# Kernel optimization log

Hardware: AMD Instinct MI355X
Metric: run time of the kernel (lower is better)

Reference implementation:

```python
import jax, jax.numpy as jnp
import numpy as np

B, N, C, H = 4, 1024, 512, 8
HD = C // H
SCALE = HD ** -0.5
LN_EPS = 1e-5


def setup_inputs() -> dict:
    key = jax.random.key(0)
    ks = jax.random.split(key, 4)
    return {
        "x": jax.random.normal(ks[0], (B, N, C), dtype=jnp.float32),
        "Wqkv": jax.random.normal(ks[1], (C, 3 * C), dtype=jnp.float32) * (C ** -0.5),
        "bqkv": jnp.zeros((3 * C,), dtype=jnp.float32),
        "order_weights": jnp.ones((3,), dtype=jnp.float32),
        "Wproj": jax.random.normal(ks[2], (C, C), dtype=jnp.float32) * (C ** -0.5),
        "bproj": jnp.zeros((C,), dtype=jnp.float32),
        "gamma": jnp.ones((C,), dtype=jnp.float32),
        "beta": jnp.zeros((C,), dtype=jnp.float32),
    }


def reference(x, Wqkv, bqkv, order_weights, Wproj, bproj, gamma, beta):
    b, n, c = x.shape
    qkv = (x @ Wqkv + bqkv).reshape(b, n, 3, H, HD)
    qkv = jnp.transpose(qkv, (2, 0, 3, 1, 4))  # [3, B, H, N, HD]
    q, k, v = qkv[0], qkv[1], qkv[2]

    base = jnp.einsum('bhnd,bhmd->bhnm', q, k) * SCALE  # [B, H, N, N]

    ow = jax.nn.softmax(order_weights)
    # torch loop: term_0 = base, term_i = base**(i+1)
    attn = ow[0] * base
    cur = base
    for i in range(1, order_weights.shape[0]):
        cur = cur * base
        attn = attn + ow[i] * cur

    attn_final = jax.nn.softmax(attn, axis=-1)

    out = jnp.einsum('bhnm,bhmd->bhnd', attn_final, v)
    out = jnp.transpose(out, (0, 2, 1, 3)).reshape(b, n, c)
    out = out @ Wproj + bproj

    y = x + out
    mu = jnp.mean(y, axis=-1, keepdims=True)
    var = jnp.var(y, axis=-1, keepdims=True)
    y = (y - mu) / jnp.sqrt(var + LN_EPS) * gamma + beta
    return y, attn_final
```

## Files before the change

kernel.cpp:

```cpp
#include <hip/hip_runtime.h>
#include <math.h>

#define B_ 4
#define N_ 1024
#define C_ 512
#define H_ 8
#define HD_ 64
#define SCALE_ 0.125f
#define LN_EPS_ 1e-5f

typedef _Float16 f16x8 __attribute__((ext_vector_type(8)));
typedef float f32x4 __attribute__((ext_vector_type(4)));

__device__ __forceinline__ void cvt_split(const float4& A, const float4& Bv,
                                          f16x8& hi, f16x8& lo) {
    float v[8] = {A.x, A.y, A.z, A.w, Bv.x, Bv.y, Bv.z, Bv.w};
#pragma unroll
    for (int i = 0; i < 8; ++i) {
        _Float16 h = (_Float16)v[i];
        hi[i] = h;
        lo[i] = (_Float16)(v[i] - (float)h);
    }
}

__global__ __launch_bounds__(256) void qkv_gemm(const float* __restrict__ x,
                                                const float* __restrict__ Wqkv,
                                                const float* __restrict__ bqkv,
                                                float* __restrict__ qkv) {
    const int K = C_;
    const int NN = 3 * C_;
    __shared__ float As[64][17];
    __shared__ float Bs[16][64];

    const int tid = threadIdx.x;
    const int tx = tid & 15;
    const int ty = tid >> 4;
    const int row0 = blockIdx.y * 64;
    const int col0 = blockIdx.x * 64;

    float acc[4][4] = {};

    for (int kt = 0; kt < K; kt += 16) {
        {
            int lin = tid * 4;
            int m = lin >> 4;
            int k = lin & 15;
            float4 a = *(const float4*)&x[(size_t)(row0 + m) * K + kt + k];
            As[m][k + 0] = a.x; As[m][k + 1] = a.y;
            As[m][k + 2] = a.z; As[m][k + 3] = a.w;
        }
        {
            int lin = tid * 4;
            int kk = lin >> 6;
            int n = lin & 63;
            *(float4*)&Bs[kk][n] =
                *(const float4*)&Wqkv[(size_t)(kt + kk) * NN + col0 + n];
        }
        __syncthreads();
#pragma unroll
        for (int kk = 0; kk < 16; ++kk) {
            float a[4], bb[4];
#pragma unroll
            for (int i = 0; i < 4; ++i) a[i] = As[ty * 4 + i][kk];
#pragma unroll
            for (int j = 0; j < 4; ++j) bb[j] = Bs[kk][tx * 4 + j];
#pragma unroll
            for (int i = 0; i < 4; ++i)
#pragma unroll
                for (int j = 0; j < 4; ++j) acc[i][j] += a[i] * bb[j];
        }
        __syncthreads();
    }
#pragma unroll
    for (int i = 0; i < 4; ++i) {
        int r = row0 + ty * 4 + i;
        int c = col0 + tx * 4;
        float4 o;
        o.x = acc[i][0] + bqkv[c + 0];
        o.y = acc[i][1] + bqkv[c + 1];
        o.z = acc[i][2] + bqkv[c + 2];
        o.w = acc[i][3] + bqkv[c + 3];
        *(float4*)&qkv[(size_t)r * NN + c] = o;
    }
}

__global__ __launch_bounds__(256) void attn_scores(const float* __restrict__ qkv,
                                                   const float* __restrict__ ow_in,
                                                   float* __restrict__ attn) {
    __shared__ float smax[4][16];
    __shared__ float ssum[4][16];

    const int tid = threadIdx.x;
    const int lane = tid & 63;
    const int w = tid >> 6;
    const int r16 = lane & 15;
    const int g = lane >> 4;
    const int n0 = blockIdx.x * 16;
    const int bh = blockIdx.y;
    const int b = bh >> 3, h = bh & 7;
    const size_t RS = 3 * C_;

    float w0 = ow_in[0], w1 = ow_in[1], w2 = ow_in[2];
    float wm = fmaxf(w0, fmaxf(w1, w2));
    float e0 = __expf(w0 - wm), e1 = __expf(w1 - wm), e2 = __expf(w2 - wm);
    float einv = 1.0f / (e0 + e1 + e2);
    float ow0 = e0 * einv, ow1 = e1 * einv, ow2 = e2 * einv;

    const float* qrow = qkv + (size_t)(b * N_ + n0 + r16) * RS + h * HD_;
    f16x8 aHi0, aLo0, aHi1, aLo1;
    {
        float4 qa = ((const float4*)qrow)[2 * g + 0];
        float4 qb = ((const float4*)qrow)[2 * g + 1];
        float4 qc = ((const float4*)qrow)[8 + 2 * g];
        float4 qd = ((const float4*)qrow)[9 + 2 * g];
        cvt_split(qa, qb, aHi0, aLo0);
        cvt_split(qc, qd, aHi1, aLo1);
    }

    float p[16][4];

    const float* kbase = qkv + (size_t)(b * N_) * RS + C_ + h * HD_;
#pragma unroll
    for (int t = 0; t < 16; ++t) {
        const int ct = w * 16 + t;
        const float* krow = kbase + (size_t)(ct * 16 + r16) * RS;
        float4 ka = ((const float4*)krow)[2 * g + 0];
        float4 kb = ((const float4*)krow)[2 * g + 1];
        float4 kc = ((const float4*)krow)[8 + 2 * g];
        float4 kd = ((const float4*)krow)[9 + 2 * g];
        f16x8 bHi0, bLo0, bHi1, bLo1;
        cvt_split(ka, kb, bHi0, bLo0);
        cvt_split(kc, kd, bHi1, bLo1);

        f32x4 acc = {0.f, 0.f, 0.f, 0.f};
        acc = __builtin_amdgcn_mfma_f32_16x16x32_f16(aHi0, bHi0, acc, 0, 0, 0);
        acc = __builtin_amdgcn_mfma_f32_16x16x32_f16(aHi0, bLo0, acc, 0, 0, 0);
        acc = __builtin_amdgcn_mfma_f32_16x16x32_f16(aLo0, bHi0, acc, 0, 0, 0);
        acc = __builtin_amdgcn_mfma_f32_16x16x32_f16(aHi1, bHi1, acc, 0, 0, 0);
        acc = __builtin_amdgcn_mfma_f32_16x16x32_f16(aHi1, bLo1, acc, 0, 0, 0);
        acc = __builtin_amdgcn_mfma_f32_16x16x32_f16(aLo1, bHi1, acc, 0, 0, 0);

#pragma unroll
        for (int j = 0; j < 4; ++j) {
            float s = acc[j] * SCALE_;
            p[t][j] = s * (ow0 + s * (ow1 + s * ow2));
        }
    }

    float rmax[4] = {-1e30f, -1e30f, -1e30f, -1e30f};
#pragma unroll
    for (int t = 0; t < 16; ++t)
#pragma unroll
        for (int j = 0; j < 4; ++j) rmax[j] = fmaxf(rmax[j], p[t][j]);
#pragma unroll
    for (int j = 0; j < 4; ++j)
#pragma unroll
        for (int m = 1; m < 16; m <<= 1)
            rmax[j] = fmaxf(rmax[j], __shfl_xor(rmax[j], m, 64));
    if (r16 == 0) {
#pragma unroll
        for (int j = 0; j < 4; ++j) smax[w][g * 4 + j] = rmax[j];
    }
    __syncthreads();
    float gm[4];
#pragma unroll
    for (int j = 0; j < 4; ++j) {
        int rr = g * 4 + j;
        gm[j] = fmaxf(fmaxf(smax[0][rr], smax[1][rr]),
                      fmaxf(smax[2][rr], smax[3][rr]));
    }

    float rsum[4] = {0.f, 0.f, 0.f, 0.f};
#pragma unroll
    for (int t = 0; t < 16; ++t)
#pragma unroll
        for (int j = 0; j < 4; ++j) {
            float e = __expf(p[t][j] - gm[j]);
            p[t][j] = e;
            rsum[j] += e;
        }
#pragma unroll
    for (int j = 0; j < 4; ++j)
#pragma unroll
        for (int m = 1; m < 16; m <<= 1)
            rsum[j] += __shfl_xor(rsum[j], m, 64);
    if (r16 == 0) {
#pragma unroll
        for (int j = 0; j < 4; ++j) ssum[w][g * 4 + j] = rsum[j];
    }
    __syncthreads();
    float inv[4];
#pragma unroll
    for (int j = 0; j < 4; ++j) {
        int rr = g * 4 + j;
        inv[j] = 1.0f / (ssum[0][rr] + ssum[1][rr] + ssum[2][rr] + ssum[3][rr]);
    }

    float* abase = attn + ((size_t)bh * N_ + n0 + 4 * g) * N_ + w * 256 + r16;
#pragma unroll
    for (int j = 0; j < 4; ++j) {
        float* arow = abase + (size_t)j * N_;
        float sc = inv[j];
#pragma unroll
        for (int t = 0; t < 16; ++t)
            arow[t * 16] = p[t][j] * sc;
    }
}

__global__ __launch_bounds__(256) void pv_gemm(const float* __restrict__ qkv,
                                               const float* __restrict__ attn,
                                               float* __restrict__ ctx) {
    __shared__ __align__(16) float Pst[64][68];
    __shared__ __align__(16) float Vs[64][68];

    const int tid = threadIdx.x;
    const int tx = tid & 15;
    const int ty = tid >> 4;
    const int n0 = blockIdx.x * 64;
    const int bh = blockIdx.y;
    const int b = bh >> 3, h = bh & 7;
    const size_t RS = 3 * C_;

    const int rr = tid >> 2;
    const int q = tid & 3;

    float acc[4][4] = {};

    for (int mt = 0; mt < 16; ++mt) {
        const int m0 = mt * 64;
        const float* prow = attn + ((size_t)bh * N_ + n0 + rr) * N_ + m0 + q * 16;
        const float* vrow = qkv + (size_t)(b * N_ + m0 + rr) * RS + 2 * C_ + h * HD_ + q * 16;
        float4 pv[4], vv[4];
#pragma unroll
        for (int m = 0; m < 4; ++m) pv[m] = ((const float4*)prow)[m];
#pragma unroll
        for (int m = 0; m < 4; ++m) vv[m] = ((const float4*)vrow)[m];
        __syncthreads();
#pragma unroll
        for (int m = 0; m < 4; ++m) {
            int c = q * 16 + m * 4;
            Pst[c + 0][rr] = pv[m].x; Pst[c + 1][rr] = pv[m].y;
            Pst[c + 2][rr] = pv[m].z; Pst[c + 3][rr] = pv[m].w;
            *(float4*)&Vs[rr][c] = vv[m];
        }
        __syncthreads();
#pragma unroll 16
        for (int mm = 0; mm < 64; ++mm) {
            float4 a4 = *(const float4*)&Pst[mm][ty * 4];
            float4 b4 = *(const float4*)&Vs[mm][tx * 4];
            float a[4] = {a4.x, a4.y, a4.z, a4.w};
            float bb[4] = {b4.x, b4.y, b4.z, b4.w};
#pragma unroll
            for (int i = 0; i < 4; ++i)
#pragma unroll
                for (int j = 0; j < 4; ++j) acc[i][j] += a[i] * bb[j];
        }
    }
#pragma unroll
    for (int i = 0; i < 4; ++i) {
        float4 o;
        o.x = acc[i][0]; o.y = acc[i][1]; o.z = acc[i][2]; o.w = acc[i][3];
        *(float4*)&ctx[(size_t)(b * N_ + n0 + ty * 4 + i) * C_ + h * HD_ + tx * 4] = o;
    }
}

__global__ __launch_bounds__(256) void proj_gemm(const float* __restrict__ ctx,
                                                 const float* __restrict__ x,
                                                 const float* __restrict__ Wproj,
                                                 const float* __restrict__ bproj,
                                                 float* __restrict__ y) {
    const int K = C_;
    const int NN = C_;
    __shared__ float As[64][17];
    __shared__ float Bs[16][64];

    const int tid = threadIdx.x;
    const int tx = tid & 15;
    const int ty = tid >> 4;
    const int row0 = blockIdx.y * 64;
    const int col0 = blockIdx.x * 64;

    float acc[4][4] = {};

    for (int kt = 0; kt < K; kt += 16) {
        {
            int lin = tid * 4;
            int m = lin >> 4;
            int k = lin & 15;
            float4 a = *(const float4*)&ctx[(size_t)(row0 + m) * K + kt + k];
            As[m][k + 0] = a.x; As[m][k + 1] = a.y;
            As[m][k + 2] = a.z; As[m][k + 3] = a.w;
        }
        {
            int lin = tid * 4;
            int kk = lin >> 6;
            int n = lin & 63;
            *(float4*)&Bs[kk][n] =
                *(const float4*)&Wproj[(size_t)(kt + kk) * NN + col0 + n];
        }
        __syncthreads();
#pragma unroll
        for (int kk = 0; kk < 16; ++kk) {
            float a[4], bb[4];
#pragma unroll
            for (int i = 0; i < 4; ++i) a[i] = As[ty * 4 + i][kk];
#pragma unroll
            for (int j = 0; j < 4; ++j) bb[j] = Bs[kk][tx * 4 + j];
#pragma unroll
            for (int i = 0; i < 4; ++i)
#pragma unroll
                for (int j = 0; j < 4; ++j) acc[i][j] += a[i] * bb[j];
        }
        __syncthreads();
    }
#pragma unroll
    for (int i = 0; i < 4; ++i) {
        int r = row0 + ty * 4 + i;
        int c = col0 + tx * 4;
        float4 xr = *(const float4*)&x[(size_t)r * C_ + c];
        float4 o;
        o.x = acc[i][0] + bproj[c + 0] + xr.x;
        o.y = acc[i][1] + bproj[c + 1] + xr.y;
        o.z = acc[i][2] + bproj[c + 2] + xr.z;
        o.w = acc[i][3] + bproj[c + 3] + xr.w;
        *(float4*)&y[(size_t)r * C_ + c] = o;
    }
}

__global__ __launch_bounds__(256) void ln_kernel(float* __restrict__ y,
                                                 const float* __restrict__ gamma,
                                                 const float* __restrict__ beta) {
    __shared__ float wsum[4], wsq[4];
    const int row = blockIdx.x;
    const int tid = threadIdx.x;
    const int lane = tid & 63;
    const int w = tid >> 6;

    float2 v = ((const float2*)(y + (size_t)row * C_))[tid];
    float s = v.x + v.y;
    float sq = v.x * v.x + v.y * v.y;
#pragma unroll
    for (int m = 1; m < 64; m <<= 1) {
        s += __shfl_xor(s, m, 64);
        sq += __shfl_xor(sq, m, 64);
    }
    if (lane == 0) { wsum[w] = s; wsq[w] = sq; }
    __syncthreads();
    float ts = wsum[0] + wsum[1] + wsum[2] + wsum[3];
    float tq = wsq[0] + wsq[1] + wsq[2] + wsq[3];
    float mu = ts * (1.0f / C_);
    float var = tq * (1.0f / C_) - mu * mu;
    float rstd = rsqrtf(var + LN_EPS_);

    float2 g = ((const float2*)gamma)[tid];
    float2 be = ((const float2*)beta)[tid];
    float2 o;
    o.x = (v.x - mu) * rstd * g.x + be.x;
    o.y = (v.y - mu) * rstd * g.y + be.y;
    ((float2*)(y + (size_t)row * C_))[tid] = o;
}

extern "C" void kernel_launch(void* const* d_in, const int* in_sizes, int n_in,
                              void* d_out, int out_size, void* d_ws, size_t ws_size,
                              hipStream_t stream) {
    const float* x     = (const float*)d_in[0];
    const float* Wqkv  = (const float*)d_in[1];
    const float* bqkv  = (const float*)d_in[2];
    const float* ow    = (const float*)d_in[3];
    const float* Wproj = (const float*)d_in[4];
    const float* bproj = (const float*)d_in[5];
    const float* gamma = (const float*)d_in[6];
    const float* beta  = (const float*)d_in[7];

    float* out  = (float*)d_out;
    float* y    = out;
    float* attn = out + (size_t)B_ * N_ * C_;
    float* qkv  = (float*)d_ws;
    float* ctx  = qkv + (size_t)B_ * N_ * 3 * C_;

    dim3 g1(3 * C_ / 64, B_ * N_ / 64);
    qkv_gemm<<<g1, 256, 0, stream>>>(x, Wqkv, bqkv, qkv);

    dim3 g2(N_ / 16, B_ * H_);
    attn_scores<<<g2, 256, 0, stream>>>(qkv, ow, attn);

    dim3 g3(N_ / 64, B_ * H_);
    pv_gemm<<<g3, 256, 0, stream>>>(qkv, attn, ctx);

    dim3 g4(C_ / 64, B_ * N_ / 64);
    proj_gemm<<<g4, 256, 0, stream>>>(ctx, x, Wproj, bproj, y);

    ln_kernel<<<B_ * N_, 256, 0, stream>>>(y, gamma, beta);
}
```

Measured before the change: 441.1 us.

## Replace scalar FP32 QKV GEMM with split-FP16 MFMA using pre-transposed weights

Adds a pre-pass kernel that transposes Wqkv and splits it into high and low FP16 parts, stored temporarily in the attn output buffer before attn_scores overwrites it. The QKV projection then runs on MFMA 16x16x32 f16 instructions, using three products (hi*hi, hi*lo, lo*hi) to approximate FP32 accuracy. The aim is to replace the scalar FMA shared-memory GEMM with matrix-core throughput. In exchange it adds an extra launch and weight conversion on every call, loads operands directly from global memory without LDS staging, and writes outputs with scattered scalar stores.

```diff
diff --git a/kernel.cpp b/kernel.cpp
--- a/kernel.cpp
+++ b/kernel.cpp
@@ -23,65 +23,86 @@
     }
 }
 
-__global__ __launch_bounds__(256) void qkv_gemm(const float* __restrict__ x,
-                                                const float* __restrict__ Wqkv,
-                                                const float* __restrict__ bqkv,
-                                                float* __restrict__ qkv) {
-    const int K = C_;
-    const int NN = 3 * C_;
-    __shared__ float As[64][17];
-    __shared__ float Bs[16][64];
-
-    const int tid = threadIdx.x;
-    const int tx = tid & 15;
-    const int ty = tid >> 4;
-    const int row0 = blockIdx.y * 64;
-    const int col0 = blockIdx.x * 64;
-
-    float acc[4][4] = {};
-
-    for (int kt = 0; kt < K; kt += 16) {
+__global__ __launch_bounds__(256) void wsplit_qkv(const float* __restrict__ W,
+                                                  _Float16* __restrict__ wt_hi,
+                                                  _Float16* __restrict__ wt_lo) {
+    __shared__ float tile[64][65];
+    const int tid = threadIdx.x;
+    const int n0 = blockIdx.x * 64;
+    const int k0 = blockIdx.y * 64;
+#pragma unroll
+    for (int i = 0; i < 16; ++i) {
+        int e = tid + i * 256;
+        int kk = e >> 6, nn = e & 63;
+        tile[kk][nn] = W[(size_t)(k0 + kk) * (3 * C_) + n0 + nn];
+    }
+    __syncthreads();
+#pragma unroll
+    for (int i = 0; i < 16; ++i) {
+        int e = tid + i * 256;
+        int n = e >> 6, k = e & 63;
+        float v = tile[k][n];
+        _Float16 h = (_Float16)v;
+        wt_hi[(size_t)(n0 + n) * C_ + k0 + k] = h;
+        wt_lo[(size_t)(n0 + n) * C_ + k0 + k] = (_Float16)(v - (float)h);
+    }
+}
+
+__global__ __launch_bounds__(256) void qkv_gemm_mfma(const float* __restrict__ x,
+                                                     const _Float16* __restrict__ wt_hi,
+                                                     const _Float16* __restrict__ wt_lo,
+                                                     const float* __restrict__ bqkv,
+                                                     float* __restrict__ qkv) {
+    const int tid = threadIdx.x;
+    const int lane = tid & 63;
+    const int w = tid >> 6;
+    const int r16 = lane & 15;
+    const int g = lane >> 4;
+    const int row0 = blockIdx.x * 32;
+    const int col0 = blockIdx.y * 256 + w * 64;
+
+    f32x4 acc[2][4] = {};
+
+    const float* xr0 = x + (size_t)(row0 + r16) * C_;
+    const float* xr1 = x + (size_t)(row0 + 16 + r16) * C_;
+
+    for (int kt = 0; kt < 16; ++kt) {
+        const int k0 = kt * 32 + 8 * g;
+        f16x8 aHi0, aLo0, aHi1, aLo1;
         {
-            int lin = tid * 4;
-            int m = lin >> 4;
-            int k = lin & 15;
-            float4 a = *(const float4*)&x[(size_t)(row0 + m) * K + kt + k];
-            As[m][k + 0] = a.x; As[m][k + 1] = a.y;
-            As[m][k + 2] = a.z; As[m][k + 3] = a.w;
-        }
-        {
-            int lin = tid * 4;
-            int kk = lin >> 6;
-            int n = lin & 63;
-            *(float4*)&Bs[kk][n] =
-                *(const float4*)&Wqkv[(size_t)(kt + kk) * NN + col0 + n];
-        }
-        __syncthreads();
-#pragma unroll
-        for (int kk = 0; kk < 16; ++kk) {
-            float a[4], bb[4];
-#pragma unroll
-            for (int i = 0; i < 4; ++i) a[i] = As[ty * 4 + i][kk];
-#pragma unroll
-            for (int j = 0; j < 4; ++j) bb[j] = Bs[kk][tx * 4 + j];
-#pragma unroll
-            for (int i = 0; i < 4; ++i)
-#pragma unroll
-                for (int j = 0; j < 4; ++j) acc[i][j] += a[i] * bb[j];
-        }
-        __syncthreads();
-    }
-#pragma unroll
-    for (int i = 0; i < 4; ++i) {
-        int r = row0 + ty * 4 + i;
-        int c = col0 + tx * 4;
-        float4 o;
-        o.x = acc[i][0] + bqkv[c + 0];
-        o.y = acc[i][1] + bqkv[c + 1];
-        o.z = acc[i][2] + bqkv[c + 2];
-        o.w = acc[i][3] + bqkv[c + 3];
-        *(float4*)&qkv[(size_t)r * NN + c] = o;
-    }
+            float4 a0 = *(const float4*)&xr0[k0];
+            float4 a1 = *(const float4*)&xr0[k0 + 4];
+            cvt_split(a0, a1, aHi0, aLo0);
+            float4 b0 = *(const float4*)&xr1[k0];
+            float4 b1 = *(const float4*)&xr1[k0 + 4];
+            cvt_split(b0, b1, aHi1, aLo1);
+        }
+#pragma unroll
+        for (int ct = 0; ct < 4; ++ct) {
+            const int c = col0 + ct * 16 + r16;
+            f16x8 bHi = *(const f16x8*)&wt_hi[(size_t)c * C_ + k0];
+            f16x8 bLo = *(const f16x8*)&wt_lo[(size_t)c * C_ + k0];
+            acc[0][ct] = __builtin_amdgcn_mfma_f32_16x16x32_f16(aHi0, bHi, acc[0][ct], 0, 0, 0);
+            acc[0][ct] = __builtin_amdgcn_mfma_f32_16x16x32_f16(aHi0, bLo, acc[0][ct], 0, 0, 0);
+            acc[0][ct] = __builtin_amdgcn_mfma_f32_16x16x32_f16(aLo0, bHi, acc[0][ct], 0, 0, 0);
+            acc[1][ct] = __builtin_amdgcn_mfma_f32_16x16x32_f16(aHi1, bHi, acc[1][ct], 0, 0, 0);
+            acc[1][ct] = __builtin_amdgcn_mfma_f32_16x16x32_f16(aHi1, bLo, acc[1][ct], 0, 0, 0);
+            acc[1][ct] = __builtin_amdgcn_mfma_f32_16x16x32_f16(aLo1, bHi, acc[1][ct], 0, 0, 0);
+        }
+    }
+
+#pragma unroll
+    for (int rt = 0; rt < 2; ++rt)
+#pragma unroll
+        for (int ct = 0; ct < 4; ++ct) {
+            const int c = col0 + ct * 16 + r16;
+            const float bias = bqkv[c];
+#pragma unroll
+            for (int j = 0; j < 4; ++j) {
+                const int r = row0 + rt * 16 + 4 * g + j;
+                qkv[(size_t)r * (3 * C_) + c] = acc[rt][ct][j] + bias;
+            }
+        }
 }
 
 __global__ __launch_bounds__(256) void attn_scores(const float* __restrict__ qkv,
@@ -378,8 +399,14 @@
     float* qkv  = (float*)d_ws;
     float* ctx  = qkv + (size_t)B_ * N_ * 3 * C_;
 
-    dim3 g1(3 * C_ / 64, B_ * N_ / 64);
-    qkv_gemm<<<g1, 256, 0, stream>>>(x, Wqkv, bqkv, qkv);
+    _Float16* wt_hi = (_Float16*)attn;
+    _Float16* wt_lo = wt_hi + (size_t)(3 * C_) * C_;
+
+    dim3 g0(3 * C_ / 64, C_ / 64);
+    wsplit_qkv<<<g0, 256, 0, stream>>>(Wqkv, wt_hi, wt_lo);
+
+    dim3 g1(B_ * N_ / 32, 3 * C_ / 256);
+    qkv_gemm_mfma<<<g1, 256, 0, stream>>>(x, wt_hi, wt_lo, bqkv, qkv);
 
     dim3 g2(N_ / 16, B_ * H_);
     attn_scores<<<g2, 256, 0, stream>>>(qkv, ow, attn);
```

Measured after the change: 417.4 us. 5.4% less time.
